# Kernel optimization log

Measured on AMD Instinct MI355X. Metric: run time of the kernel, lower is better.

Reference implementation:

```python
import jax, jax.numpy as jnp
import numpy as np

B, C, H, W = 8, 64, 64, 64  # module requires c == h == w due to view/permute quirk


def setup_inputs() -> dict:
    key = jax.random.key(0)
    ks = jax.random.split(key, 5)
    return {
        "x": jax.random.normal(ks[0], (B, C, H, W), dtype=jnp.float32),
        "w_qkv": jax.random.normal(ks[1], (3 * C, C), dtype=jnp.float32) * (1.0 / np.sqrt(C)),
        "b_qkv": jax.random.normal(ks[2], (3 * C,), dtype=jnp.float32) * 0.02,
        "w_out": jax.random.normal(ks[3], (C, C), dtype=jnp.float32) * (1.0 / np.sqrt(C)),
        "b_out": jax.random.normal(ks[4], (C,), dtype=jnp.float32) * 0.02,
    }


def reference(x, w_qkv, b_qkv, w_out, b_out):
    b, c, h, w = x.shape
    # 1x1 conv == channel matmul (norm='none' -> Identity, the only runnable branch)
    qkv = jnp.einsum('bchw,oc->bohw', x, w_qkv) + b_qkv[None, :, None, None]
    q, k, v = jnp.split(qkv, 3, axis=1)  # each (b, c, h, w)

    def flat(t):  # (b,c,h,w) -> (b, h*w, c), matches permute(0,2,3,1).view
        return t.transpose(0, 2, 3, 1).reshape(b, h * w, c)

    q, k, v = flat(q), flat(k), flat(v)
    scale = 1.0 / jnp.sqrt(jnp.asarray(c, dtype=x.dtype))
    scores = jax.nn.softmax(jnp.einsum('bqc,bkc->bqk', q, k) * scale, axis=-1)
    out = jnp.einsum('bqk,bkc->bqc', scores, v)  # (b, hw, c)
    # Faithfully replicate the original's view(b,c,h,w).permute(0,3,1,2) quirk
    out = out.reshape(b, c, h, w).transpose(0, 3, 1, 2)  # (b, w, c, h); needs c==h==w
    out = jnp.einsum('bchw,oc->bohw', out, w_out) + b_out[None, :, None, None]
    return out + x
```

## Files before the change

### kernel.cpp

```cpp
#include <hip/hip_runtime.h>
#include <hip/hip_bf16.h>
#include <stdint.h>

typedef unsigned short u16;
typedef __attribute__((ext_vector_type(8))) short bf16x8;
typedef __attribute__((ext_vector_type(4))) float f32x4;
typedef __attribute__((ext_vector_type(2))) float f32x2;
typedef __attribute__((ext_vector_type(4))) unsigned int u32x4;
typedef __attribute__((ext_vector_type(2))) unsigned int u32x2;

#define NTOK 4096
#define NT32 32

#if __has_builtin(__builtin_amdgcn_exp2f)
#define EXP2F __builtin_amdgcn_exp2f
#else
#define EXP2F exp2f
#endif

__device__ __forceinline__ f32x4 MFMA(bf16x8 a, bf16x8 b, f32x4 c) {
    return __builtin_amdgcn_mfma_f32_16x16x32_bf16(a, b, c, 0, 0, 0);
}

__device__ __forceinline__ uint32_t pk_bf16(float a, float b) {
    uint32_t d;
    asm("v_cvt_pk_bf16_f32 %0, %1, %2" : "=v"(d) : "v"(a), "v"(b));
    return d;
}

__device__ __forceinline__ void hilo_pack8(const float* v, bf16x8* h, bf16x8* l) {
    union { uint32_t u[4]; bf16x8 b; } H, L;
#pragma unroll
    for (int m = 0; m < 4; ++m) {
        const uint32_t ua = __float_as_uint(v[2*m]);
        const uint32_t ub = __float_as_uint(v[2*m+1]);
        const float la = v[2*m]   - __uint_as_float(ua & 0xffff0000u);
        const float lb = v[2*m+1] - __uint_as_float(ub & 0xffff0000u);
        H.u[m] = (ua >> 16) | (ub & 0xffff0000u);
        L.u[m] = (__float_as_uint(la) >> 16) | (__float_as_uint(lb) & 0xffff0000u);
    }
    *h = H.b; *l = L.b;
}

__global__ __launch_bounds__(256) void k_qkv(
    const float* __restrict__ x, const float* __restrict__ wqkv, const float* __restrict__ bqkv,
    u16* __restrict__ Qp, u16* __restrict__ Kp, u16* __restrict__ Vp)
{
    __shared__ float qt_lds[64 * 194];
    const int blk = blockIdx.x;
    const int b   = blk >> 6;
    const int tb  = (blk & 63) << 6;
    const int tid = threadIdx.x;
    const int lane = tid & 63;
    const int wv  = __builtin_amdgcn_readfirstlane(tid >> 6);
    const int r   = lane & 15;
    const int g   = lane >> 4;
    const int o0  = wv * 48;

    {
        const int c  = tid >> 2;
        const int t0 = (tid & 3) * 16;
        const float* xp = x + (size_t)(b * 64 + c) * NTOK + tb + t0;
#pragma unroll
        for (int m = 0; m < 4; ++m) {
            f32x4 v = *(const f32x4*)(xp + 4*m);
            *(f32x2*)&qt_lds[c*66 + t0 + 4*m]     = f32x2{v[0], v[1]};
            *(f32x2*)&qt_lds[c*66 + t0 + 4*m + 2] = f32x2{v[2], v[3]};
        }
    }

    bf16x8 wh[3][2], wl[3][2];
#pragma unroll
    for (int oi = 0; oi < 3; ++oi)
#pragma unroll
        for (int ks = 0; ks < 2; ++ks) {
            const float* wp = wqkv + (size_t)(o0 + oi*16 + r) * 64 + ks*32 + g*8;
            float wv8[8];
            *(f32x4*)(wv8)     = *(const f32x4*)(wp);
            *(f32x4*)(wv8 + 4) = *(const f32x4*)(wp + 4);
            hilo_pack8(wv8, &wh[oi][ks], &wl[oi][ks]);
        }
    __syncthreads();

    f32x4 acc[3][4];
#pragma unroll
    for (int oi = 0; oi < 3; ++oi)
#pragma unroll
        for (int tt = 0; tt < 4; ++tt) acc[oi][tt] = 0.f;

#pragma unroll
    for (int tt = 0; tt < 4; ++tt) {
        bf16x8 xh[2], xl[2];
#pragma unroll
        for (int ks = 0; ks < 2; ++ks) {
            float xv[8];
#pragma unroll
            for (int j = 0; j < 8; ++j)
                xv[j] = qt_lds[(ks*32 + g*8 + j)*66 + tt*16 + r];
            hilo_pack8(xv, &xh[ks], &xl[ks]);
        }
#pragma unroll
        for (int oi = 0; oi < 3; ++oi) {
            f32x4 a = acc[oi][tt];
            a = MFMA(wh[oi][0], xh[0], a);
            a = MFMA(wh[oi][1], xh[1], a);
            a = MFMA(wl[oi][0], xh[0], a);
            a = MFMA(wl[oi][1], xh[1], a);
            a = MFMA(wh[oi][0], xl[0], a);
            a = MFMA(wh[oi][1], xl[1], a);
            acc[oi][tt] = a;
        }
    }
    __syncthreads();

#pragma unroll
    for (int oi = 0; oi < 3; ++oi)
#pragma unroll
        for (int tt = 0; tt < 4; ++tt)
#pragma unroll
            for (int i = 0; i < 4; ++i)
                qt_lds[(tt*16 + r) * 194 + o0 + oi*16 + g*4 + i] = acc[oi][tt][i];
    __syncthreads();

    const float SC = 0.18033688011112042f;

    {
        const int t = tid >> 2, c0 = (tid & 3) * 16;
        float v[16], bq[16];
#pragma unroll
        for (int m = 0; m < 8; ++m)
            *(f32x2*)(v + 2*m) = *(const f32x2*)&qt_lds[t*194 + c0 + 2*m];
#pragma unroll
        for (int m = 0; m < 4; ++m)
            *(f32x4*)(bq + 4*m) = *(const f32x4*)(bqkv + c0 + 4*m);
        u32x4 P0, P1;
#pragma unroll
        for (int m = 0; m < 4; ++m) {
            P0[m] = pk_bf16((v[2*m]   + bq[2*m]  ) * SC, (v[2*m+1] + bq[2*m+1]) * SC);
            P1[m] = pk_bf16((v[8+2*m] + bq[8+2*m]) * SC, (v[9+2*m] + bq[9+2*m]) * SC);
        }
        size_t base = ((size_t)(b * NTOK + tb + t)) * 64 + c0;
        *(u32x4*)(Qp + base)     = P0;
        *(u32x4*)(Qp + base + 8) = P1;
    }

#pragma unroll
    for (int uu = 0; uu < 2; ++uu) {
        const int u  = tid * 2 + uu;
        const int t  = u >> 3;
        const int ks = (u >> 2) & 1;
        const int gk = u & 3;
        const int cb0 = 64 + ks*32 + gk*8;
        float v[8];
#pragma unroll
        for (int m = 0; m < 4; ++m)
            *(f32x2*)(v + 2*m) = *(const f32x2*)&qt_lds[t*194 + cb0 + 2*m];
        u32x4 P;
#pragma unroll
        for (int m = 0; m < 4; ++m)
            P[m] = pk_bf16(v[2*m] + bqkv[cb0 + 2*m], v[2*m+1] + bqkv[cb0 + 2*m+1]);
        const int tg = tb + t;
        size_t kbase = (size_t)b * 262144 + ((size_t)(tg >> 4) * 2 + ks) * 512 + gk*128 + (t & 15) * 8;
        *(u32x4*)(Kp + kbase) = P;
    }

    {
        const int cb = (tid >> 4) & 3;
        const int r2 = tid & 15;
        const float bv = bqkv[128 + cb*16 + r2];
        const int T = (blk & 63) >> 1;
        const int halfb = blk & 1;
#pragma unroll
        for (int m = 0; m < 4; ++m) {
            const int tq = m * 4 + (tid >> 6);
            float v[4];
#pragma unroll
            for (int jj = 0; jj < 4; ++jj)
                v[jj] = qt_lds[(tq*4 + jj)*194 + 128 + cb*16 + r2] + bv;
            const int t = tq * 4;
            const int wtr = halfb*2 + (t >> 5);
            const int sti = (t >> 4) & 1;
            const int g2  = (t >> 2) & 3;
            u32x2 W;
            W[0] = pk_bf16(v[0], v[1]);
            W[1] = pk_bf16(v[2], v[3]);
            size_t vbase = (size_t)b * 262144 +
                           (((size_t)T * 4 + wtr) * 4 + cb) * 512 + (g2*16 + r2) * 8 + sti * 4;
            *(u32x2*)(Vp + vbase) = W;
        }
    }
}

__global__ __launch_bounds__(256, 2) void k_attn(
    const u16* __restrict__ Qp, const u16* __restrict__ Kp, const u16* __restrict__ Vp,
    const float* __restrict__ wout, const float* __restrict__ bout,
    const float* __restrict__ x, float* __restrict__ out)
{
    __shared__ float larr[4][64];
    __shared__ float otbuf[2][64 * 67];
    const int hw  = blockIdx.x;
    const int b   = hw & 7;
    const int qt  = hw >> 3;
    const int tid = threadIdx.x;
    const int lane = tid & 63;
    const int wt2 = tid >> 6;
    const int r   = lane & 15;
    const int g   = lane >> 4;
    const int row0 = qt * 64;

    bf16x8 qh[4][2];
#pragma unroll
    for (int rt = 0; rt < 4; ++rt) {
        const size_t qoff = ((size_t)(b * NTOK + row0 + rt*16 + r)) * 64 + g * 8;
        qh[rt][0] = *(const bf16x8*)(Qp + qoff);
        qh[rt][1] = *(const bf16x8*)(Qp + qoff + 32);
    }

    const u16* kbase = Kp + (size_t)b * 262144 + wt2 * 2048 + (size_t)lane * 8;
    const u16* vptr  = Vp + (size_t)b * 262144 + wt2 * 2048 + (size_t)lane * 8;

    bf16x8 ONES;
#pragma unroll
    for (int j = 0; j < 8; ++j) ONES[j] = (short)0x3F80;

    f32x4 oacc[4][4];
#pragma unroll
    for (int rt = 0; rt < 4; ++rt)
#pragma unroll
        for (int cb = 0; cb < 4; ++cb) oacc[rt][cb] = 0.f;
    f32x4 lacc[4];
#pragma unroll
    for (int rt = 0; rt < 4; ++rt) lacc[rt] = 0.f;

    bf16x8 kA[2][2], kB[2][2];
#pragma unroll
    for (int sti = 0; sti < 2; ++sti)
#pragma unroll
        for (int ks = 0; ks < 2; ++ks) {
            kA[sti][ks] = *(const bf16x8*)(kbase + (size_t)0*8192 + sti*1024 + ks*512);
            kB[sti][ks] = *(const bf16x8*)(kbase + (size_t)1*8192 + sti*1024 + ks*512);
        }

    auto halfrt = [&](bf16x8 (&kb)[2][2], bf16x8 (&vf)[4], int rt0) {
        f32x4 s[2][2];
        __builtin_amdgcn_s_setprio(1);
#pragma unroll
        for (int rr = 0; rr < 2; ++rr)
#pragma unroll
            for (int sti = 0; sti < 2; ++sti) {
                f32x4 a = {0.f, 0.f, 0.f, 0.f};
                a = MFMA(kb[sti][0], qh[rt0 + rr][0], a);
                a = MFMA(kb[sti][1], qh[rt0 + rr][1], a);
                s[rr][sti] = a;
            }
        __builtin_amdgcn_s_setprio(0);

#pragma unroll
        for (int rr = 0; rr < 2; ++rr) {
            const int rt = rt0 + rr;
            float p[8];
#pragma unroll
            for (int sti = 0; sti < 2; ++sti)
#pragma unroll
                for (int i = 0; i < 4; ++i)
                    p[sti*4 + i] = EXP2F(s[rr][sti][i]);
            union { uint32_t u[4]; bf16x8 b; } PA;
#pragma unroll
            for (int m = 0; m < 4; ++m) PA.u[m] = pk_bf16(p[2*m], p[2*m+1]);
            __builtin_amdgcn_s_setprio(1);
#pragma unroll
            for (int cb = 0; cb < 4; ++cb)
                oacc[rt][cb] = MFMA(PA.b, vf[cb], oacc[rt][cb]);
            lacc[rt] = MFMA(PA.b, ONES, lacc[rt]);
            __builtin_amdgcn_s_setprio(0);
        }
    };

    auto body = [&](bf16x8 (&kb)[2][2], int Tp) {
        bf16x8 vf[4];
#pragma unroll
        for (int cb = 0; cb < 4; ++cb)
            vf[cb] = *(const bf16x8*)(vptr + cb*512);
        vptr += 8192;

        halfrt(kb, vf, 0);
        halfrt(kb, vf, 2);

        const u16* kp = kbase + (size_t)Tp * 8192;
#pragma unroll
        for (int sti = 0; sti < 2; ++sti)
#pragma unroll
            for (int ks = 0; ks < 2; ++ks)
                kb[sti][ks] = *(const bf16x8*)(kp + sti*1024 + ks*512);
    };

    for (int T = 0; T < NT32; T += 2) {
        const int TpA = (T + 2 < NT32) ? T + 2 : NT32 - 1;
        const int TpB = (T + 3 < NT32) ? T + 3 : NT32 - 1;
        body(kA, TpA);
        body(kB, TpB);
    }

    if (r == 0) {
#pragma unroll
        for (int rt = 0; rt < 4; ++rt)
#pragma unroll
            for (int i = 0; i < 4; ++i)
                larr[wt2][rt*16 + g*4 + i] = lacc[rt][i];
    }

    if (wt2 < 2) {
        float* ob = otbuf[wt2];
#pragma unroll
        for (int rt = 0; rt < 4; ++rt)
#pragma unroll
            for (int cb = 0; cb < 4; ++cb)
#pragma unroll
                for (int i = 0; i < 4; ++i)
                    ob[(rt*16 + g*4 + i)*67 + cb*16 + r] = oacc[rt][cb][i];
    }
    __syncthreads();
    if (wt2 >= 2) {
        float* ob = otbuf[wt2 - 2];
#pragma unroll
        for (int rt = 0; rt < 4; ++rt)
#pragma unroll
            for (int cb = 0; cb < 4; ++cb)
#pragma unroll
                for (int i = 0; i < 4; ++i)
                    ob[(rt*16 + g*4 + i)*67 + cb*16 + r] += oacc[rt][cb][i];
    }
    __syncthreads();

    const int orow = wt2*16 + r;
    const float inv = 1.0f / (larr[0][orow] + larr[1][orow] + larr[2][orow] + larr[3][orow]);
    bf16x8 oh_[2], ol_[2];
#pragma unroll
    for (int ks = 0; ks < 2; ++ks) {
        float ov[8];
#pragma unroll
        for (int j = 0; j < 8; ++j) {
            const int idx = orow*67 + ks*32 + g*8 + j;
            ov[j] = (otbuf[0][idx] + otbuf[1][idx]) * inv;
        }
        hilo_pack8(ov, &oh_[ks], &ol_[ks]);
    }
#pragma unroll
    for (int ot = 0; ot < 4; ++ot) {
        bf16x8 wh2[2], wl2[2];
#pragma unroll
        for (int ks = 0; ks < 2; ++ks) {
            const float* wp = wout + (size_t)(ot*16 + r) * 64 + ks*32 + g*8;
            float wv8[8];
            *(f32x4*)(wv8)     = *(const f32x4*)(wp);
            *(f32x4*)(wv8 + 4) = *(const f32x4*)(wp + 4);
            hilo_pack8(wv8, &wh2[ks], &wl2[ks]);
        }
        f32x4 a = {0.f, 0.f, 0.f, 0.f};
        a = MFMA(wh2[0], oh_[0], a);
        a = MFMA(wh2[1], oh_[1], a);
        a = MFMA(wl2[0], oh_[0], a);
        a = MFMA(wl2[1], oh_[1], a);
        a = MFMA(wh2[0], ol_[0], a);
        a = MFMA(wh2[1], ol_[1], a);
#pragma unroll
        for (int i = 0; i < 4; ++i) {
            const int oo = ot*16 + g*4 + i;
            const size_t xi = ((size_t)(b*64 + oo)) * NTOK + row0 + wt2*16 + r;
            out[xi] = a[i] + bout[oo] + x[xi];
        }
    }
}

extern "C" void kernel_launch(void* const* d_in, const int* in_sizes, int n_in,
                              void* d_out, int out_size, void* d_ws, size_t ws_size,
                              hipStream_t stream)
{
    (void)in_sizes; (void)n_in; (void)out_size; (void)ws_size;
    const float* x    = (const float*)d_in[0];
    const float* wqkv = (const float*)d_in[1];
    const float* bqkv = (const float*)d_in[2];
    const float* wout = (const float*)d_in[3];
    const float* bout = (const float*)d_in[4];
    float* out = (float*)d_out;

    char* ws = (char*)d_ws;
    const size_t MB = 1024 * 1024;
    u16* Qp = (u16*)(ws);
    u16* Kp = (u16*)(ws + 4 * MB);
    u16* Vp = (u16*)(ws + 8 * MB);

    k_qkv<<<512, 256, 0, stream>>>(x, wqkv, bqkv, Qp, Kp, Vp);
    k_attn<<<512, 256, 0, stream>>>(Qp, Kp, Vp, wout, bout, x, out);
}
```

Measured before the change: 54.06 us.

## Split attention over key halves and combine partials in separate output kernel

Each attention block now processes only half of the key/value tiles, doubling the grid to 1024 blocks. Unnormalized partial outputs and row sums are written to workspace. A new kernel sums the two halves, normalizes, and applies the output projection, bias and residual. The intent is to raise occupancy and parallelism, at the cost of an extra launch and roughly 16 MB of extra global traffic.

```diff
diff --git a/kernel.cpp b/kernel.cpp
--- a/kernel.cpp
+++ b/kernel.cpp
@@ -10,7 +10,7 @@
 typedef __attribute__((ext_vector_type(2))) unsigned int u32x2;
 
 #define NTOK 4096
-#define NT32 32
+#define NTHALF 16
 
 #if __has_builtin(__builtin_amdgcn_exp2f)
 #define EXP2F __builtin_amdgcn_exp2f
@@ -193,11 +193,167 @@
 
 __global__ __launch_bounds__(256, 2) void k_attn(
     const u16* __restrict__ Qp, const u16* __restrict__ Kp, const u16* __restrict__ Vp,
+    float* __restrict__ Opart, float* __restrict__ Lpart)
+{
+    __shared__ float larr[4][64];
+    __shared__ float otbuf[2][64 * 67];
+    const int hw  = blockIdx.x;
+    const int b   = hw & 7;
+    const int rest = hw >> 3;
+    const int qt  = rest >> 1;
+    const int kh  = rest & 1;
+    const int tid = threadIdx.x;
+    const int lane = tid & 63;
+    const int wt2 = tid >> 6;
+    const int r   = lane & 15;
+    const int g   = lane >> 4;
+    const int row0 = qt * 64;
+
+    bf16x8 qh[4][2];
+#pragma unroll
+    for (int rt = 0; rt < 4; ++rt) {
+        const size_t qoff = ((size_t)(b * NTOK + row0 + rt*16 + r)) * 64 + g * 8;
+        qh[rt][0] = *(const bf16x8*)(Qp + qoff);
+        qh[rt][1] = *(const bf16x8*)(Qp + qoff + 32);
+    }
+
+    const u16* kbase = Kp + (size_t)b * 262144 + (size_t)kh * NTHALF * 8192 + wt2 * 2048 + (size_t)lane * 8;
+    const u16* vptr  = Vp + (size_t)b * 262144 + (size_t)kh * NTHALF * 8192 + wt2 * 2048 + (size_t)lane * 8;
+
+    bf16x8 ONES;
+#pragma unroll
+    for (int j = 0; j < 8; ++j) ONES[j] = (short)0x3F80;
+
+    f32x4 oacc[4][4];
+#pragma unroll
+    for (int rt = 0; rt < 4; ++rt)
+#pragma unroll
+        for (int cb = 0; cb < 4; ++cb) oacc[rt][cb] = 0.f;
+    f32x4 lacc[4];
+#pragma unroll
+    for (int rt = 0; rt < 4; ++rt) lacc[rt] = 0.f;
+
+    bf16x8 kA[2][2], kB[2][2];
+#pragma unroll
+    for (int sti = 0; sti < 2; ++sti)
+#pragma unroll
+        for (int ks = 0; ks < 2; ++ks) {
+            kA[sti][ks] = *(const bf16x8*)(kbase + (size_t)0*8192 + sti*1024 + ks*512);
+            kB[sti][ks] = *(const bf16x8*)(kbase + (size_t)1*8192 + sti*1024 + ks*512);
+        }
+
+    auto halfrt = [&](bf16x8 (&kb)[2][2], bf16x8 (&vf)[4], int rt0) {
+        f32x4 s[2][2];
+        __builtin_amdgcn_s_setprio(1);
+#pragma unroll
+        for (int rr = 0; rr < 2; ++rr)
+#pragma unroll
+            for (int sti = 0; sti < 2; ++sti) {
+                f32x4 a = {0.f, 0.f, 0.f, 0.f};
+                a = MFMA(kb[sti][0], qh[rt0 + rr][0], a);
+                a = MFMA(kb[sti][1], qh[rt0 + rr][1], a);
+                s[rr][sti] = a;
+            }
+        __builtin_amdgcn_s_setprio(0);
+
+#pragma unroll
+        for (int rr = 0; rr < 2; ++rr) {
+            const int rt = rt0 + rr;
+            float p[8];
+#pragma unroll
+            for (int sti = 0; sti < 2; ++sti)
+#pragma unroll
+                for (int i = 0; i < 4; ++i)
+                    p[sti*4 + i] = EXP2F(s[rr][sti][i]);
+            union { uint32_t u[4]; bf16x8 b; } PA;
+#pragma unroll
+            for (int m = 0; m < 4; ++m) PA.u[m] = pk_bf16(p[2*m], p[2*m+1]);
+            __builtin_amdgcn_s_setprio(1);
+#pragma unroll
+            for (int cb = 0; cb < 4; ++cb)
+                oacc[rt][cb] = MFMA(PA.b, vf[cb], oacc[rt][cb]);
+            lacc[rt] = MFMA(PA.b, ONES, lacc[rt]);
+            __builtin_amdgcn_s_setprio(0);
+        }
+    };
+
+    auto body = [&](bf16x8 (&kb)[2][2], int Tp) {
+        bf16x8 vf[4];
+#pragma unroll
+        for (int cb = 0; cb < 4; ++cb)
+            vf[cb] = *(const bf16x8*)(vptr + cb*512);
+        vptr += 8192;
+
+        halfrt(kb, vf, 0);
+        halfrt(kb, vf, 2);
+
+        const u16* kp = kbase + (size_t)Tp * 8192;
+#pragma unroll
+        for (int sti = 0; sti < 2; ++sti)
+#pragma unroll
+            for (int ks = 0; ks < 2; ++ks)
+                kb[sti][ks] = *(const bf16x8*)(kp + sti*1024 + ks*512);
+    };
+
+    for (int T = 0; T < NTHALF; T += 2) {
+        const int TpA = (T + 2 < NTHALF) ? T + 2 : NTHALF - 1;
+        const int TpB = (T + 3 < NTHALF) ? T + 3 : NTHALF - 1;
+        body(kA, TpA);
+        body(kB, TpB);
+    }
+
+    if (r == 0) {
+#pragma unroll
+        for (int rt = 0; rt < 4; ++rt)
+#pragma unroll
+            for (int i = 0; i < 4; ++i)
+                larr[wt2][rt*16 + g*4 + i] = lacc[rt][i];
+    }
+
+    if (wt2 < 2) {
+        float* ob = otbuf[wt2];
+#pragma unroll
+        for (int rt = 0; rt < 4; ++rt)
+#pragma unroll
+            for (int cb = 0; cb < 4; ++cb)
+#pragma unroll
+                for (int i = 0; i < 4; ++i)
+                    ob[(rt*16 + g*4 + i)*67 + cb*16 + r] = oacc[rt][cb][i];
+    }
+    __syncthreads();
+    if (wt2 >= 2) {
+        float* ob = otbuf[wt2 - 2];
+#pragma unroll
+        for (int rt = 0; rt < 4; ++rt)
+#pragma unroll
+            for (int cb = 0; cb < 4; ++cb)
+#pragma unroll
+                for (int i = 0; i < 4; ++i)
+                    ob[(rt*16 + g*4 + i)*67 + cb*16 + r] += oacc[rt][cb][i];
+    }
+    __syncthreads();
+
+    float* OB = Opart + (((size_t)(b * 64 + qt)) * 2 + kh) * 4096;
+    {
+        const int row = tid >> 2, c0 = (tid & 3) * 16;
+#pragma unroll
+        for (int m = 0; m < 4; ++m) {
+            f32x4 v0 = *(const f32x4*)&otbuf[0][row*67 + c0 + 4*m];
+            f32x4 v1 = *(const f32x4*)&otbuf[1][row*67 + c0 + 4*m];
+            *(f32x4*)&OB[row*64 + c0 + 4*m] = v0 + v1;
+        }
+    }
+    if (tid < 64) {
+        Lpart[(((size_t)(b * 64 + qt)) * 2 + kh) * 64 + tid] =
+            larr[0][tid] + larr[1][tid] + larr[2][tid] + larr[3][tid];
+    }
+}
+
+__global__ __launch_bounds__(256) void k_out(
+    const float* __restrict__ Opart, const float* __restrict__ Lpart,
     const float* __restrict__ wout, const float* __restrict__ bout,
     const float* __restrict__ x, float* __restrict__ out)
 {
-    __shared__ float larr[4][64];
-    __shared__ float otbuf[2][64 * 67];
     const int hw  = blockIdx.x;
     const int b   = hw & 7;
     const int qt  = hw >> 3;
@@ -208,140 +364,25 @@
     const int g   = lane >> 4;
     const int row0 = qt * 64;
 
-    bf16x8 qh[4][2];
-#pragma unroll
-    for (int rt = 0; rt < 4; ++rt) {
-        const size_t qoff = ((size_t)(b * NTOK + row0 + rt*16 + r)) * 64 + g * 8;
-        qh[rt][0] = *(const bf16x8*)(Qp + qoff);
-        qh[rt][1] = *(const bf16x8*)(Qp + qoff + 32);
-    }
-
-    const u16* kbase = Kp + (size_t)b * 262144 + wt2 * 2048 + (size_t)lane * 8;
-    const u16* vptr  = Vp + (size_t)b * 262144 + wt2 * 2048 + (size_t)lane * 8;
-
-    bf16x8 ONES;
-#pragma unroll
-    for (int j = 0; j < 8; ++j) ONES[j] = (short)0x3F80;
-
-    f32x4 oacc[4][4];
-#pragma unroll
-    for (int rt = 0; rt < 4; ++rt)
-#pragma unroll
-        for (int cb = 0; cb < 4; ++cb) oacc[rt][cb] = 0.f;
-    f32x4 lacc[4];
-#pragma unroll
-    for (int rt = 0; rt < 4; ++rt) lacc[rt] = 0.f;
-
-    bf16x8 kA[2][2], kB[2][2];
-#pragma unroll
-    for (int sti = 0; sti < 2; ++sti)
-#pragma unroll
-        for (int ks = 0; ks < 2; ++ks) {
-            kA[sti][ks] = *(const bf16x8*)(kbase + (size_t)0*8192 + sti*1024 + ks*512);
-            kB[sti][ks] = *(const bf16x8*)(kbase + (size_t)1*8192 + sti*1024 + ks*512);
-        }
-
-    auto halfrt = [&](bf16x8 (&kb)[2][2], bf16x8 (&vf)[4], int rt0) {
-        f32x4 s[2][2];
-        __builtin_amdgcn_s_setprio(1);
-#pragma unroll
-        for (int rr = 0; rr < 2; ++rr)
-#pragma unroll
-            for (int sti = 0; sti < 2; ++sti) {
-                f32x4 a = {0.f, 0.f, 0.f, 0.f};
-                a = MFMA(kb[sti][0], qh[rt0 + rr][0], a);
-                a = MFMA(kb[sti][1], qh[rt0 + rr][1], a);
-                s[rr][sti] = a;
-            }
-        __builtin_amdgcn_s_setprio(0);
-
-#pragma unroll
-        for (int rr = 0; rr < 2; ++rr) {
-            const int rt = rt0 + rr;
-            float p[8];
-#pragma unroll
-            for (int sti = 0; sti < 2; ++sti)
-#pragma unroll
-                for (int i = 0; i < 4; ++i)
-                    p[sti*4 + i] = EXP2F(s[rr][sti][i]);
-            union { uint32_t u[4]; bf16x8 b; } PA;
-#pragma unroll
-            for (int m = 0; m < 4; ++m) PA.u[m] = pk_bf16(p[2*m], p[2*m+1]);
-            __builtin_amdgcn_s_setprio(1);
-#pragma unroll
-            for (int cb = 0; cb < 4; ++cb)
-                oacc[rt][cb] = MFMA(PA.b, vf[cb], oacc[rt][cb]);
-            lacc[rt] = MFMA(PA.b, ONES, lacc[rt]);
-            __builtin_amdgcn_s_setprio(0);
-        }
-    };
-
-    auto body = [&](bf16x8 (&kb)[2][2], int Tp) {
-        bf16x8 vf[4];
-#pragma unroll
-        for (int cb = 0; cb < 4; ++cb)
-            vf[cb] = *(const bf16x8*)(vptr + cb*512);
-        vptr += 8192;
-
-        halfrt(kb, vf, 0);
-        halfrt(kb, vf, 2);
-
-        const u16* kp = kbase + (size_t)Tp * 8192;
-#pragma unroll
-        for (int sti = 0; sti < 2; ++sti)
-#pragma unroll
-            for (int ks = 0; ks < 2; ++ks)
-                kb[sti][ks] = *(const bf16x8*)(kp + sti*1024 + ks*512);
-    };
-
-    for (int T = 0; T < NT32; T += 2) {
-        const int TpA = (T + 2 < NT32) ? T + 2 : NT32 - 1;
-        const int TpB = (T + 3 < NT32) ? T + 3 : NT32 - 1;
-        body(kA, TpA);
-        body(kB, TpB);
-    }
-
-    if (r == 0) {
-#pragma unroll
-        for (int rt = 0; rt < 4; ++rt)
-#pragma unroll
-            for (int i = 0; i < 4; ++i)
-                larr[wt2][rt*16 + g*4 + i] = lacc[rt][i];
-    }
-
-    if (wt2 < 2) {
-        float* ob = otbuf[wt2];
-#pragma unroll
-        for (int rt = 0; rt < 4; ++rt)
-#pragma unroll
-            for (int cb = 0; cb < 4; ++cb)
-#pragma unroll
-                for (int i = 0; i < 4; ++i)
-                    ob[(rt*16 + g*4 + i)*67 + cb*16 + r] = oacc[rt][cb][i];
-    }
-    __syncthreads();
-    if (wt2 >= 2) {
-        float* ob = otbuf[wt2 - 2];
-#pragma unroll
-        for (int rt = 0; rt < 4; ++rt)
-#pragma unroll
-            for (int cb = 0; cb < 4; ++cb)
-#pragma unroll
-                for (int i = 0; i < 4; ++i)
-                    ob[(rt*16 + g*4 + i)*67 + cb*16 + r] += oacc[rt][cb][i];
-    }
-    __syncthreads();
+    const float* O0 = Opart + ((size_t)(b * 64 + qt)) * 2 * 4096;
+    const float* O1 = O0 + 4096;
+    const float* L  = Lpart + ((size_t)(b * 64 + qt)) * 2 * 64;
 
     const int orow = wt2*16 + r;
-    const float inv = 1.0f / (larr[0][orow] + larr[1][orow] + larr[2][orow] + larr[3][orow]);
+    const float inv = 1.0f / (L[orow] + L[64 + orow]);
+
     bf16x8 oh_[2], ol_[2];
 #pragma unroll
     for (int ks = 0; ks < 2; ++ks) {
         float ov[8];
-#pragma unroll
-        for (int j = 0; j < 8; ++j) {
-            const int idx = orow*67 + ks*32 + g*8 + j;
-            ov[j] = (otbuf[0][idx] + otbuf[1][idx]) * inv;
+        f32x4 a0 = *(const f32x4*)&O0[orow*64 + ks*32 + g*8];
+        f32x4 a1 = *(const f32x4*)&O0[orow*64 + ks*32 + g*8 + 4];
+        f32x4 b0 = *(const f32x4*)&O1[orow*64 + ks*32 + g*8];
+        f32x4 b1 = *(const f32x4*)&O1[orow*64 + ks*32 + g*8 + 4];
+#pragma unroll
+        for (int i = 0; i < 4; ++i) {
+            ov[i]     = (a0[i] + b0[i]) * inv;
+            ov[4 + i] = (a1[i] + b1[i]) * inv;
         }
         hilo_pack8(ov, &oh_[ks], &ol_[ks]);
     }
@@ -386,10 +427,13 @@
 
     char* ws = (char*)d_ws;
     const size_t MB = 1024 * 1024;
-    u16* Qp = (u16*)(ws);
-    u16* Kp = (u16*)(ws + 4 * MB);
-    u16* Vp = (u16*)(ws + 8 * MB);
+    u16*   Qp    = (u16*)(ws);
+    u16*   Kp    = (u16*)(ws + 4 * MB);
+    u16*   Vp    = (u16*)(ws + 8 * MB);
+    float* Opart = (float*)(ws + 12 * MB);
+    float* Lpart = (float*)(ws + 29 * MB);
 
     k_qkv<<<512, 256, 0, stream>>>(x, wqkv, bqkv, Qp, Kp, Vp);
-    k_attn<<<512, 256, 0, stream>>>(Qp, Kp, Vp, wout, bout, x, out);
-}
+    k_attn<<<1024, 256, 0, stream>>>(Qp, Kp, Vp, Opart, Lpart);
+    k_out<<<512, 256, 0, stream>>>(Opart, Lpart, wout, bout, x, out);
+}
```

New measurement: 59.80 us. 10.6% more time.
